# Kernel tuning notes

Hardware: AMD Instinct MI355X
Metric: run time of the kernel (lower is better)

Reference implementation:

```python
import jax, jax.numpy as jnp
import numpy as np

H = 48        # num attention heads
D = 128       # head dim
KV = 1        # multi-query: single KV head


def setup_inputs() -> dict:
    key = jax.random.key(0)
    ks = jax.random.split(key, 5)
    B, S, HID = 1, 2048, 6144
    QKV_OUT = HID + 2 * KV * D  # 6400
    scale = 0.02
    return {
        "x": jax.random.normal(ks[0], (B, S, HID), jnp.float32),
        "wqkv": jax.random.normal(ks[1], (QKV_OUT, HID), jnp.float32) * scale,
        "bqkv": jax.random.normal(ks[2], (QKV_OUT,), jnp.float32) * scale,
        "wo": jax.random.normal(ks[3], (HID, HID), jnp.float32) * scale,
        "bo": jax.random.normal(ks[4], (HID,), jnp.float32) * scale,
    }


def reference(x, wqkv, bqkv, wo, bo):
    B, S, HID = x.shape
    # fused QKV projection (c_attn), bias=True
    qkv = jnp.einsum('bsh,oh->bso', x, wqkv) + bqkv          # [B,S,6400]
    q = qkv[..., :HID].reshape(B, S, H, D)                    # [B,S,H,D]
    k = qkv[..., HID:HID + KV * D].reshape(B, S, D)           # [B,S,D] (single KV head)
    v = qkv[..., HID + KV * D:].reshape(B, S, D)              # [B,S,D]

    # multi-query causal attention: all H query heads attend to the one KV head
    scores = jnp.einsum('bqhd,bkd->bhqk', q, k) * (1.0 / np.sqrt(D).astype(np.float32))
    causal = jnp.tril(jnp.ones((S, S), dtype=bool))
    scores = jnp.where(causal[None, None], scores, jnp.finfo(scores.dtype).min)
    probs = jax.nn.softmax(scores, axis=-1)                   # [B,H,S,S]
    attn = jnp.einsum('bhqk,bkd->bqhd', probs, v)             # [B,S,H,D]
    attn = attn.reshape(B, S, H * D)                          # [B,S,HID]

    # output projection (c_proj), bias added (bias_pre_add semantics are TP-only)
    return jnp.einsum('bsh,oh->bso', attn, wo) + bo
```

## Files before the change

### kernel.cpp

```cpp
#include <hip/hip_runtime.h>
#include <hip/hip_bf16.h>
#include <cstdint>
#include <cstddef>

#define SEQ  2048
#define HID_ 6144
#define NKV  6400
#define NH_  48
#define HD_  128

typedef unsigned short u16;
typedef __bf16 bf16x8 __attribute__((ext_vector_type(8)));
typedef float  f32x4  __attribute__((ext_vector_type(4)));
typedef unsigned short us8 __attribute__((ext_vector_type(8)));

__device__ __forceinline__ void async_ld16(const void* g, void* l) {
  __builtin_amdgcn_global_load_lds(
      (const __attribute__((address_space(1))) unsigned int*)g,
      (__attribute__((address_space(3))) unsigned int*)l, 16, 0, 0);
}

__device__ __forceinline__ u16 f2b(float f) {
  __hip_bfloat16 h = __float2bfloat16(f);
  return *reinterpret_cast<u16*>(&h);
}

__global__ void cvt_f32_bf16(const float* __restrict__ in, u16* __restrict__ out,
                             long n8) {
  const long i = (long)blockIdx.x * blockDim.x + threadIdx.x;
  if (i >= n8) return;
  const long o = i * 8;
  const float4 f0 = *(const float4*)(in + o);
  const float4 f1 = *(const float4*)(in + o + 4);
  us8 v;
  v[0] = f2b(f0.x); v[1] = f2b(f0.y); v[2] = f2b(f0.z); v[3] = f2b(f0.w);
  v[4] = f2b(f1.x); v[5] = f2b(f1.y); v[6] = f2b(f1.z); v[7] = f2b(f1.w);
  *(us8*)(out + o) = v;
}

template <int N, int K, typename OT>
__global__ __launch_bounds__(256, 2)
void gemm_bt_bias(const u16* __restrict__ A, const u16* __restrict__ B,
                  const float* __restrict__ bias, OT* __restrict__ C) {
  __shared__ u16 As[128 * 32];
  __shared__ u16 Bs[128 * 32];
  const int tid  = threadIdx.x;
  const int lane = tid & 63, wave = tid >> 6;
  const int l15  = lane & 15, quad = lane >> 4;
  const int wm = wave >> 1, wn = wave & 1;
  const int m0 = blockIdx.y * 128, n0 = blockIdx.x * 128;

  f32x4 acc[4][4];
#pragma unroll
  for (int i = 0; i < 4; ++i)
#pragma unroll
    for (int j = 0; j < 4; ++j) acc[i][j] = f32x4{0.f, 0.f, 0.f, 0.f};

  const int rowA0 = tid >> 2, col8 = (tid & 3) * 8;
  const u16* gA = A + (size_t)(m0 + rowA0) * K + col8;
  const u16* gB = B + (size_t)(n0 + rowA0) * K + col8;
  u16* lA = As + tid * 8;
  u16* lB = Bs + tid * 8;

  for (int k0 = 0; k0 < K; k0 += 32) {
    async_ld16(gA + k0, lA);
    async_ld16(gA + (size_t)64 * K + k0, lA + 256 * 8);
    async_ld16(gB + k0, lB);
    async_ld16(gB + (size_t)64 * K + k0, lB + 256 * 8);
    __syncthreads();

    const u16* aBase = As + (wm * 64 + l15) * 32 + quad * 8;
    const u16* bBase = Bs + (wn * 64 + l15) * 32 + quad * 8;
    bf16x8 af[4], bfr[4];
#pragma unroll
    for (int i = 0; i < 4; ++i) {
      af[i]  = *(const bf16x8*)(aBase + i * 16 * 32);
      bfr[i] = *(const bf16x8*)(bBase + i * 16 * 32);
    }
#pragma unroll
    for (int i = 0; i < 4; ++i)
#pragma unroll
      for (int j = 0; j < 4; ++j)
        acc[i][j] = __builtin_amdgcn_mfma_f32_16x16x32_bf16(af[i], bfr[j], acc[i][j], 0, 0, 0);
    __syncthreads();
  }

#pragma unroll
  for (int j = 0; j < 4; ++j) {
    const int n = n0 + wn * 64 + j * 16 + l15;
    const float bv = bias[n];
#pragma unroll
    for (int i = 0; i < 4; ++i) {
      const int mrow = m0 + wm * 64 + i * 16 + quad * 4;
#pragma unroll
      for (int r = 0; r < 4; ++r) {
        const float v = acc[i][j][r] + bv;
        if constexpr (sizeof(OT) == 2)
          C[(size_t)(mrow + r) * N + n] = (OT)f2b(v);
        else
          C[(size_t)(mrow + r) * N + n] = (OT)v;
      }
    }
  }
}

__global__ __launch_bounds__(256, 3)
void mqa_flash(const u16* __restrict__ qkv, u16* __restrict__ attn) {
  __shared__ u16 Ks[4 * 64 * 32];
  __shared__ u16 Vt[128 * 72];
  __shared__ u16 Ps[4 * 16 * 72];
  const int tid  = threadIdx.x;
  const int lane = tid & 63, wave = tid >> 6;
  const int l15  = lane & 15, quad = lane >> 4;
  const int h  = blockIdx.x;
  const int qb = (int)gridDim.y - 1 - (int)blockIdx.y;
  const int q0 = qb * 64;
  const float scale = 0.088388347648318447f;

  bf16x8 qf[4];
  {
    const u16* qp = qkv + (size_t)(q0 + wave * 16 + l15) * NKV + h * HD_ + quad * 8;
#pragma unroll
    for (int kc = 0; kc < 4; ++kc) qf[kc] = *(const bf16x8*)(qp + kc * 32);
  }

  f32x4 oacc[8];
#pragma unroll
  for (int nd = 0; nd < 8; ++nd) oacc[nd] = f32x4{0.f, 0.f, 0.f, 0.f};
  float mrun[4], lrun[4];
#pragma unroll
  for (int r = 0; r < 4; ++r) { mrun[r] = -1e30f; lrun[r] = 0.f; }

  const int krow = tid >> 2, kc8 = (tid & 3) * 8;
  const int kv2 = lane & 31;
  const int dg  = wave * 2 + (lane >> 5);

  auto load_tile = [&](int t, us8* kr, us8* vr) {
    const int kv0 = t * 64;
    const u16* kp = qkv + (size_t)(kv0 + krow) * NKV + HID_ + kc8;
#pragma unroll
    for (int r = 0; r < 4; ++r) kr[r] = *(const us8*)(kp + r * 32);
    const u16* vp = qkv + (size_t)(kv0 + kv2 * 2) * NKV + HID_ + HD_ + dg * 16;
    vr[0] = *(const us8*)(vp);
    vr[1] = *(const us8*)(vp + 8);
    vr[2] = *(const us8*)(vp + NKV);
    vr[3] = *(const us8*)(vp + NKV + 8);
  };

  auto stage_tile = [&](const us8* kr, const us8* vr) {
    u16* kd = Ks + tid * 8;
#pragma unroll
    for (int r = 0; r < 4; ++r) *(us8*)(kd + r * 2048) = kr[r];
#pragma unroll
    for (int i = 0; i < 8; ++i) {
      unsigned v0 = (unsigned)vr[0][i] | ((unsigned)vr[2][i] << 16);
      unsigned v1 = (unsigned)vr[1][i] | ((unsigned)vr[3][i] << 16);
      *(unsigned*)(Vt + (dg * 16 + i) * 72 + kv2 * 2) = v0;
      *(unsigned*)(Vt + (dg * 16 + 8 + i) * 72 + kv2 * 2) = v1;
    }
  };

  auto compute_tile = [&](int t) {
    const int kv0 = t * 64;
    f32x4 s[4];
#pragma unroll
    for (int nt = 0; nt < 4; ++nt) {
      f32x4 c4 = f32x4{0.f, 0.f, 0.f, 0.f};
#pragma unroll
      for (int kc = 0; kc < 4; ++kc) {
        bf16x8 kf = *(const bf16x8*)(Ks + kc * 2048 + (nt * 16 + l15) * 32 + quad * 8);
        c4 = __builtin_amdgcn_mfma_f32_16x16x32_bf16(qf[kc], kf, c4, 0, 0, 0);
      }
      s[nt] = c4;
    }

    float mt[4] = {-1e30f, -1e30f, -1e30f, -1e30f};
    if (t == qb) {
#pragma unroll
      for (int nt = 0; nt < 4; ++nt) {
        const int kvg = kv0 + nt * 16 + l15;
#pragma unroll
        for (int r = 0; r < 4; ++r) {
          const int qg = q0 + wave * 16 + quad * 4 + r;
          float v = s[nt][r] * scale;
          v = (kvg <= qg) ? v : -1e30f;
          s[nt][r] = v;
          mt[r] = fmaxf(mt[r], v);
        }
      }
    } else {
#pragma unroll
      for (int nt = 0; nt < 4; ++nt)
#pragma unroll
        for (int r = 0; r < 4; ++r) {
          const float v = s[nt][r] * scale;
          s[nt][r] = v;
          mt[r] = fmaxf(mt[r], v);
        }
    }
#pragma unroll
    for (int off = 1; off < 16; off <<= 1)
#pragma unroll
      for (int r = 0; r < 4; ++r) mt[r] = fmaxf(mt[r], __shfl_xor(mt[r], off));

    float alpha[4], rsum[4];
#pragma unroll
    for (int r = 0; r < 4; ++r) {
      const float mnew = fmaxf(mrun[r], mt[r]);
      alpha[r] = __expf(mrun[r] - mnew);
      mrun[r] = mnew;
      rsum[r] = 0.f;
    }
    u16* pw = Ps + wave * (16 * 72);
#pragma unroll
    for (int nt = 0; nt < 4; ++nt)
#pragma unroll
      for (int r = 0; r < 4; ++r) {
        const float p = __expf(s[nt][r] - mrun[r]);
        rsum[r] += p;
        pw[(quad * 4 + r) * 72 + nt * 16 + l15] = f2b(p);
      }
#pragma unroll
    for (int off = 1; off < 16; off <<= 1)
#pragma unroll
      for (int r = 0; r < 4; ++r) rsum[r] += __shfl_xor(rsum[r], off);
#pragma unroll
    for (int r = 0; r < 4; ++r) lrun[r] = lrun[r] * alpha[r] + rsum[r];
#pragma unroll
    for (int nd = 0; nd < 8; ++nd)
#pragma unroll
      for (int r = 0; r < 4; ++r) oacc[nd][r] *= alpha[r];

#pragma unroll
    for (int kc2 = 0; kc2 < 2; ++kc2) {
      bf16x8 pf = *(const bf16x8*)(pw + l15 * 72 + kc2 * 32 + quad * 8);
#pragma unroll
      for (int nd = 0; nd < 8; ++nd) {
        bf16x8 vf = *(const bf16x8*)(Vt + (nd * 16 + l15) * 72 + kc2 * 32 + quad * 8);
        oacc[nd] = __builtin_amdgcn_mfma_f32_16x16x32_bf16(pf, vf, oacc[nd], 0, 0, 0);
      }
    }
  };

  us8 kA[4], vA[4], kB[4], vB[4];
  load_tile(0, kA, vA);
  for (int t = 0; t <= qb; ++t) {
    const int tn = (t < qb) ? t + 1 : t;
    if (!(t & 1)) {
      stage_tile(kA, vA);
      load_tile(tn, kB, vB);
    } else {
      stage_tile(kB, vB);
      load_tile(tn, kA, vA);
    }
    __syncthreads();
    compute_tile(t);
    __syncthreads();
  }

#pragma unroll
  for (int r = 0; r < 4; ++r) {
    const int qg = q0 + wave * 16 + quad * 4 + r;
    const float inv = 1.f / lrun[r];
#pragma unroll
    for (int nd = 0; nd < 8; ++nd)
      attn[(size_t)qg * HID_ + h * HD_ + nd * 16 + l15] = f2b(oacc[nd][r] * inv);
  }
}

extern "C" void kernel_launch(void* const* d_in, const int* in_sizes, int n_in,
                              void* d_out, int out_size, void* d_ws, size_t ws_size,
                              hipStream_t stream) {
  const float* x    = (const float*)d_in[0];
  const float* wqkv = (const float*)d_in[1];
  const float* bqkv = (const float*)d_in[2];
  const float* wo   = (const float*)d_in[3];
  const float* bo   = (const float*)d_in[4];
  float* out = (float*)d_out;

  u16* xb     = (u16*)d_ws;
  u16* wqkvb  = xb + (size_t)SEQ * HID_;
  u16* wob    = wqkvb + (size_t)NKV * HID_;
  u16* qkvws  = wob + (size_t)HID_ * HID_;
  u16* attnws = qkvws + (size_t)SEQ * NKV;

  {
    const long n8x = (long)SEQ * HID_ / 8;
    cvt_f32_bf16<<<(n8x + 255) / 256, 256, 0, stream>>>(x, xb, n8x);
    const long n8q = (long)NKV * HID_ / 8;
    cvt_f32_bf16<<<(n8q + 255) / 256, 256, 0, stream>>>(wqkv, wqkvb, n8q);
    const long n8o = (long)HID_ * HID_ / 8;
    cvt_f32_bf16<<<(n8o + 255) / 256, 256, 0, stream>>>(wo, wob, n8o);
  }

  gemm_bt_bias<NKV, HID_, u16><<<dim3(NKV / 128, SEQ / 128), 256, 0, stream>>>(
      xb, wqkvb, bqkv, qkvws);
  mqa_flash<<<dim3(NH_, SEQ / 64), 256, 0, stream>>>(qkvws, attnws);
  gemm_bt_bias<HID_, HID_, float><<<dim3(HID_ / 128, SEQ / 128), 256, 0, stream>>>(
      attnws, wob, bo, out);
}
```

Baseline: 934.9 us.

## Rewrite GEMMs as 256x256-tile kernels with 4-stage async LDS pipeline

Replaces the 128x128 single-buffered GEMM with a 512-thread, 256x256-tile kernel that uses a 4-deep ring of async global-to-LDS loads, explicit vmcnt waits, MFMA priority boosting and a swizzled 1D block order for L2 locality. The goal is to hide global load latency behind MFMA work and raise arithmetic intensity per block. The cost is heavy LDS use (128 KB per block) and more accumulator registers, which may limit occupancy. The launch grid of 200 or 192 blocks depends on M being exactly 2048 (8 row tiles).

```diff
diff --git a/kernel.cpp b/kernel.cpp
--- a/kernel.cpp
+++ b/kernel.cpp
@@ -39,50 +39,76 @@
 }
 
 template <int N, int K, typename OT>
-__global__ __launch_bounds__(256, 2)
-void gemm_bt_bias(const u16* __restrict__ A, const u16* __restrict__ B,
-                  const float* __restrict__ bias, OT* __restrict__ C) {
-  __shared__ u16 As[128 * 32];
-  __shared__ u16 Bs[128 * 32];
+__global__ __launch_bounds__(512, 2)
+void gemm256(const u16* __restrict__ A, const u16* __restrict__ B,
+             const float* __restrict__ bias, OT* __restrict__ C) {
+  __shared__ u16 lds_[4 * 2 * 8192];
+  constexpr int NT = K / 32;
+
   const int tid  = threadIdx.x;
   const int lane = tid & 63, wave = tid >> 6;
   const int l15  = lane & 15, quad = lane >> 4;
-  const int wm = wave >> 1, wn = wave & 1;
-  const int m0 = blockIdx.y * 128, n0 = blockIdx.x * 128;
-
-  f32x4 acc[4][4];
-#pragma unroll
-  for (int i = 0; i < 4; ++i)
+  const int wm = wave >> 2, wn = wave & 3;
+
+  const int nb  = (int)gridDim.x;
+  const int cpx = nb >> 3;
+  const int swz = ((int)blockIdx.x & 7) * cpx + ((int)blockIdx.x >> 3);
+  const int by  = swz & 7;
+  const int bx  = swz >> 3;
+  const int m0 = by * 256, n0 = bx * 256;
+
+  f32x4 acc[8][4];
+#pragma unroll
+  for (int i = 0; i < 8; ++i)
 #pragma unroll
     for (int j = 0; j < 4; ++j) acc[i][j] = f32x4{0.f, 0.f, 0.f, 0.f};
 
-  const int rowA0 = tid >> 2, col8 = (tid & 3) * 8;
-  const u16* gA = A + (size_t)(m0 + rowA0) * K + col8;
-  const u16* gB = B + (size_t)(n0 + rowA0) * K + col8;
-  u16* lA = As + tid * 8;
-  u16* lB = Bs + tid * 8;
-
-  for (int k0 = 0; k0 < K; k0 += 32) {
-    async_ld16(gA + k0, lA);
-    async_ld16(gA + (size_t)64 * K + k0, lA + 256 * 8);
-    async_ld16(gB + k0, lB);
-    async_ld16(gB + (size_t)64 * K + k0, lB + 256 * 8);
-    __syncthreads();
-
-    const u16* aBase = As + (wm * 64 + l15) * 32 + quad * 8;
-    const u16* bBase = Bs + (wn * 64 + l15) * 32 + quad * 8;
-    bf16x8 af[4], bfr[4];
-#pragma unroll
-    for (int i = 0; i < 4; ++i) {
-      af[i]  = *(const bf16x8*)(aBase + i * 16 * 32);
-      bfr[i] = *(const bf16x8*)(bBase + i * 16 * 32);
-    }
-#pragma unroll
-    for (int i = 0; i < 4; ++i)
+  const int rowc = tid >> 2, col8 = (tid & 3) * 8;
+  const u16* gA0 = A + (size_t)(m0 + rowc) * K + col8;
+  const u16* gA1 = gA0 + (size_t)128 * K;
+  const u16* gB0 = B + (size_t)(n0 + rowc) * K + col8;
+  const u16* gB1 = gB0 + (size_t)128 * K;
+
+  auto stage = [&](int t) {
+    u16* s0 = lds_ + (t & 3) * 16384;
+    const int k0 = t * 32;
+    async_ld16(gA0 + k0, s0 + tid * 8);
+    async_ld16(gA1 + k0, s0 + 4096 + tid * 8);
+    async_ld16(gB0 + k0, s0 + 8192 + tid * 8);
+    async_ld16(gB1 + k0, s0 + 8192 + 4096 + tid * 8);
+  };
+
+  stage(0); stage(1); stage(2);
+
+  for (int t = 0; t < NT; ++t) {
+    if (t + 3 < NT) stage(t + 3);
+    const int rem = NT - 1 - t;
+    if (rem >= 3)      asm volatile("s_waitcnt vmcnt(12)" ::: "memory");
+    else if (rem == 2) asm volatile("s_waitcnt vmcnt(8)" ::: "memory");
+    else if (rem == 1) asm volatile("s_waitcnt vmcnt(4)" ::: "memory");
+    else               asm volatile("s_waitcnt vmcnt(0)" ::: "memory");
+    __builtin_amdgcn_s_barrier();
+    __builtin_amdgcn_sched_barrier(0);
+
+    const u16* sa = lds_ + (t & 3) * 16384 + (wm * 128 + l15) * 32 + quad * 8;
+    const u16* sb = lds_ + (t & 3) * 16384 + 8192 + (wn * 64 + l15) * 32 + quad * 8;
+    bf16x8 af[8], bfv[4];
+#pragma unroll
+    for (int i = 0; i < 8; ++i) af[i] = *(const bf16x8*)(sa + i * 512);
+#pragma unroll
+    for (int j = 0; j < 4; ++j) bfv[j] = *(const bf16x8*)(sb + j * 512);
+
+    __builtin_amdgcn_s_setprio(1);
+#pragma unroll
+    for (int i = 0; i < 8; ++i)
 #pragma unroll
       for (int j = 0; j < 4; ++j)
-        acc[i][j] = __builtin_amdgcn_mfma_f32_16x16x32_bf16(af[i], bfr[j], acc[i][j], 0, 0, 0);
-    __syncthreads();
+        acc[i][j] = __builtin_amdgcn_mfma_f32_16x16x32_bf16(af[i], bfv[j], acc[i][j], 0, 0, 0);
+    __builtin_amdgcn_s_setprio(0);
+
+    __builtin_amdgcn_sched_barrier(0);
+    __builtin_amdgcn_s_barrier();
+    __builtin_amdgcn_sched_barrier(0);
   }
 
 #pragma unroll
@@ -90,15 +116,15 @@
     const int n = n0 + wn * 64 + j * 16 + l15;
     const float bv = bias[n];
 #pragma unroll
-    for (int i = 0; i < 4; ++i) {
-      const int mrow = m0 + wm * 64 + i * 16 + quad * 4;
+    for (int i = 0; i < 8; ++i) {
+      const int mr = m0 + wm * 128 + i * 16 + quad * 4;
 #pragma unroll
       for (int r = 0; r < 4; ++r) {
         const float v = acc[i][j][r] + bv;
         if constexpr (sizeof(OT) == 2)
-          C[(size_t)(mrow + r) * N + n] = (OT)f2b(v);
+          C[(size_t)(mr + r) * N + n] = (OT)f2b(v);
         else
-          C[(size_t)(mrow + r) * N + n] = (OT)v;
+          C[(size_t)(mr + r) * N + n] = (OT)v;
       }
     }
   }
@@ -293,9 +319,7 @@
     cvt_f32_bf16<<<(n8o + 255) / 256, 256, 0, stream>>>(wo, wob, n8o);
   }
 
-  gemm_bt_bias<NKV, HID_, u16><<<dim3(NKV / 128, SEQ / 128), 256, 0, stream>>>(
-      xb, wqkvb, bqkv, qkvws);
+  gemm256<NKV, HID_, u16><<<dim3(200), 512, 0, stream>>>(xb, wqkvb, bqkv, qkvws);
   mqa_flash<<<dim3(NH_, SEQ / 64), 256, 0, stream>>>(qkvws, attnws);
-  gemm_bt_bias<HID_, HID_, float><<<dim3(HID_ / 128, SEQ / 128), 256, 0, stream>>>(
-      attnws, wob, bo, out);
-}
+  gemm256<HID_, HID_, float><<<dim3(192), 512, 0, stream>>>(attnws, wob, bo, out);
+}
```

Result: no change. 921.8 us (-1.4%).
